# Kernel tuning notes

Hardware: AMD Instinct MI355X
Metric: run time of the kernel (lower is better)

## Reference

```python
import jax, jax.numpy as jnp
import numpy as np

N_NODES = 500_000
N_EDGES = 8_000_000
N_GRAPHS = 1000


def _mlp(x, w1, b1, w2, b2):
    # Linear -> SELU -> Linear (torch Sequential equivalent)
    return jax.nn.selu(x @ w1 + b1) @ w2 + b2


def setup_inputs() -> dict:
    key = jax.random.key(0)
    ks = jax.random.split(key, 25)
    p = lambda i, shape: jax.random.normal(ks[i], shape, jnp.float32) * 0.1
    return {
        "nodes": jax.random.normal(ks[0], (N_NODES, 1), jnp.float32),
        "edges": jax.random.normal(ks[1], (N_EDGES, 1), jnp.float32),
        "senders": jax.random.randint(ks[2], (N_EDGES,), 0, N_NODES),
        "receivers": jax.random.randint(ks[3], (N_EDGES,), 0, N_NODES),
        "graph_ids": jnp.sort(jax.random.randint(ks[4], (N_NODES,), 0, N_GRAPHS)),
        "num_graphs": N_GRAPHS,
        # permutate_nodes: 2 -> 10 -> 10
        "pn_w1": p(5, (2, 10)), "pn_b1": p(6, (10,)), "pn_w2": p(7, (10, 10)), "pn_b2": p(8, (10,)),
        # update_edges: 11 -> 5 -> 1
        "ue_w1": p(9, (11, 5)), "ue_b1": p(10, (5,)), "ue_w2": p(11, (5, 1)), "ue_b2": p(12, (1,)),
        # permutate_edges: 1 -> 5 -> 10
        "pe_w1": p(13, (1, 5)), "pe_b1": p(14, (5,)), "pe_w2": p(15, (5, 10)), "pe_b2": p(16, (10,)),
        # update_nodes: 11 -> 5 -> 1
        "un_w1": p(17, (11, 5)), "un_b1": p(18, (5,)), "un_w2": p(19, (5, 1)), "un_b2": p(20, (1,)),
        # predict: 11 -> 10 -> 10
        "pr_w1": p(21, (11, 10)), "pr_b1": p(22, (10,)), "pr_w2": p(23, (10, 10)), "pr_b2": p(24, (10,)),
    }


def reference(nodes, edges, pn_w1, pn_b1, pn_w2, pn_b2,
              ue_w1, ue_b1, ue_w2, ue_b2,
              pe_w1, pe_b1, pe_w2, pe_b2,
              un_w1, un_b1, un_w2, un_b2,
              pr_w1, pr_b1, pr_w2, pr_b2,
              senders, receivers, graph_ids, num_graphs):
    # gather node feats to edges: [recv || send] -> (E, 2)
    collected = jnp.concatenate([nodes[receivers], nodes[senders]], axis=-1)
    h1_nodes = _mlp(collected, pn_w1, pn_b1, pn_w2, pn_b2)  # (E, 10)
    h1_edges = edges  # (E, 1)
    for _ in range(3):
        h1_edges = _mlp(jnp.concatenate([h1_edges, h1_nodes], axis=-1),
                        ue_w1, ue_b1, ue_w2, ue_b2)  # (E, 1)
    # edges -> nodes aggregation (sum over receiver)
    edges_of_nodes = jax.ops.segment_sum(h1_edges, receivers, num_segments=nodes.shape[0])  # (N, 1)
    h2_edges = _mlp(edges_of_nodes, pe_w1, pe_b1, pe_w2, pe_b2)  # (N, 10)
    h2_nodes = nodes  # (N, 1)
    for _ in range(3):
        h2_nodes = _mlp(jnp.concatenate([h2_nodes, h2_edges], axis=-1),
                        un_w1, un_b1, un_w2, un_b2)  # (N, 1)
    # nodes -> globals aggregation (sum per graph)
    g = jax.ops.segment_sum(jnp.concatenate([h2_nodes, h2_edges], axis=-1),
                            graph_ids, num_segments=num_graphs)  # (G, 11)
    out = _mlp(g, pr_w1, pr_b1, pr_w2, pr_b2)  # (G, 10)
    return jax.nn.softmax(out, axis=-1)
```

## Files before the change

### kernel.cpp

```cpp
#include <hip/hip_runtime.h>
#include <hip/hip_fp16.h>
#include <math.h>

#define N_NODES_C  500000
#define N_EDGES_C  8000000
#define N_GRAPHS_C 1000
#define NGROUPS_C  (N_EDGES_C / 4)

#define BSHIFT  11
#define BWIDTH  2048
#define NBKT    245
#define BCAP    34048

#define EPB     8192
#define GPB     (EPB / 4)
#define NPB     ((N_EDGES_C + EPB - 1) / EPB)

#define GRAPH_ACC_OFF 0
#define FW_OFF        11008
#define CURSOR_OFF    11264
#define PAIRS_OFF     11520
#define WS_WORDS_NEEDED (PAIRS_OFF + NBKT * BCAP)
#define OLD_NODE_ACC_OFF 11264
#define OLD_ZERO_WORDS   (OLD_NODE_ACC_OFF + N_NODES_C)

#define LOG2E_F 1.4426950408889634f


__device__ __forceinline__ float selu2(float xl) {
    const float C1 = 0.7282901039f;
    const float C2 = 1.7580993408473766f;
    float e = __builtin_amdgcn_exp2f(xl);
    float neg = fmaf(C2, e, -C2);
    return xl > 0.0f ? C1 * xl : neg;
}

__device__ __forceinline__ float selu_f(float x) {
    const float scale = 1.0507009873554805f;
    const float sa    = 1.0507009873554805f * 1.6732632423543772f;
    float neg = sa * (__expf(x) - 1.0f);
    return x > 0.0f ? scale * x : neg;
}

__device__ __forceinline__ void atomAddF(float* p, float v) {
    __hip_atomic_fetch_add(p, v, __ATOMIC_RELAXED, __HIP_MEMORY_SCOPE_AGENT);
}

__device__ __forceinline__ void fuse_weights(
        int t,
        const float* __restrict__ pn_w1, const float* __restrict__ pn_b1,
        const float* __restrict__ pn_w2, const float* __restrict__ pn_b2,
        const float* __restrict__ ue_w1, const float* __restrict__ ue_b1,
        const float* __restrict__ ue_w2, const float* __restrict__ ue_b2,
        const float* __restrict__ pe_w1, const float* __restrict__ pe_b1,
        const float* __restrict__ pe_w2, const float* __restrict__ pe_b2,
        const float* __restrict__ un_w1, const float* __restrict__ un_b1,
        const float* __restrict__ un_w2, const float* __restrict__ un_b2,
        float* __restrict__ fw) {
    const float L = LOG2E_F;
    if (t < 20) fw[0 + t] = pn_w1[t] * L;
    if (t < 10) fw[20 + t] = pn_b1[t] * L;
    if (t < 50) {
        int j = t / 5, k = t % 5;
        float s = 0.0f;
        for (int m = 0; m < 10; ++m) s += pn_w2[j * 10 + m] * ue_w1[(1 + m) * 5 + k];
        fw[30 + t] = s * L;
    }
    if (t < 5) {
        float s = ue_b1[t];
        for (int m = 0; m < 10; ++m) s += pn_b2[m] * ue_w1[(1 + m) * 5 + t];
        fw[80 + t] = s * L;
    }
    if (t < 5)  fw[85 + t]  = ue_w1[t] * L;
    if (t < 5)  fw[90 + t]  = ue_w2[t];
    if (t == 0) fw[95]      = ue_b2[0];
    if (t < 5)  fw[96 + t]  = pe_w1[t] * L;
    if (t < 5)  fw[101 + t] = pe_b1[t] * L;
    if (t < 50) fw[106 + t] = pe_w2[t];
    if (t < 10) fw[156 + t] = pe_b2[t];
    if (t < 25) {
        int j = t / 5, k = t % 5;
        float s = 0.0f;
        for (int m = 0; m < 10; ++m) s += pe_w2[j * 10 + m] * un_w1[(1 + m) * 5 + k];
        fw[166 + t] = s * L;
    }
    if (t < 5) {
        float s = un_b1[t];
        for (int m = 0; m < 10; ++m) s += pe_b2[m] * un_w1[(1 + m) * 5 + t];
        fw[191 + t] = s * L;
    }
    if (t < 5)  fw[196 + t] = un_w1[t] * L;
    if (t < 5)  fw[201 + t] = un_w2[t];
    if (t == 0) fw[206]     = un_b2[0];
}

__global__ __launch_bounds__(256) void k_init(
        float* __restrict__ ws,
        const float* pn_w1, const float* pn_b1, const float* pn_w2, const float* pn_b2,
        const float* ue_w1, const float* ue_b1, const float* ue_w2, const float* ue_b2,
        const float* pe_w1, const float* pe_b1, const float* pe_w2, const float* pe_b2,
        const float* un_w1, const float* un_b1, const float* un_w2, const float* un_b2) {
    int i = blockIdx.x * 256 + threadIdx.x;
    if (i < 11000) ws[GRAPH_ACC_OFF + i] = 0.0f;
    if (i < 256) ((int*)ws)[CURSOR_OFF + i] = i * BCAP;
    if (blockIdx.x == 0)
        fuse_weights(threadIdx.x, pn_w1, pn_b1, pn_w2, pn_b2, ue_w1, ue_b1, ue_w2, ue_b2,
                     pe_w1, pe_b1, pe_w2, pe_b2, un_w1, un_b1, un_w2, un_b2, ws + FW_OFF);
}

__global__ void k_fuse(const float* pn_w1, const float* pn_b1, const float* pn_w2, const float* pn_b2,
                       const float* ue_w1, const float* ue_b1, const float* ue_w2, const float* ue_b2,
                       const float* pe_w1, const float* pe_b1, const float* pe_w2, const float* pe_b2,
                       const float* un_w1, const float* un_b1, const float* un_w2, const float* un_b2,
                       float* fw) {
    fuse_weights(threadIdx.x, pn_w1, pn_b1, pn_w2, pn_b2, ue_w1, ue_b1, ue_w2, ue_b2,
                 pe_w1, pe_b1, pe_w2, pe_b2, un_w1, un_b1, un_w2, un_b2, fw);
}

__global__ void k_final(const float* __restrict__ graph_acc,
                        const float* __restrict__ pr_w1, const float* __restrict__ pr_b1,
                        const float* __restrict__ pr_w2, const float* __restrict__ pr_b2,
                        float* __restrict__ out) {
    int g = blockIdx.x * blockDim.x + threadIdx.x;
    if (g >= N_GRAPHS_C) return;
    float gv[11];
#pragma unroll
    for (int f = 0; f < 11; ++f) gv[f] = graph_acc[g * 11 + f];
    float h[10];
#pragma unroll
    for (int j = 0; j < 10; ++j) {
        float z = pr_b1[j];
#pragma unroll
        for (int f = 0; f < 11; ++f) z = fmaf(gv[f], pr_w1[f * 10 + j], z);
        h[j] = selu_f(z);
    }
    float o[10];
    float mx = -1e30f;
#pragma unroll
    for (int j = 0; j < 10; ++j) {
        float z = pr_b2[j];
#pragma unroll
        for (int m = 0; m < 10; ++m) z = fmaf(h[m], pr_w2[m * 10 + j], z);
        o[j] = z;
        mx = fmaxf(mx, z);
    }
    float sum = 0.0f;
#pragma unroll
    for (int j = 0; j < 10; ++j) { o[j] = __expf(o[j] - mx); sum += o[j]; }
    float inv = 1.0f / sum;
#pragma unroll
    for (int j = 0; j < 10; ++j) out[g * 10 + j] = o[j] * inv;
}


__global__ __launch_bounds__(256) void k_part(
        const float* __restrict__ nodes, const float* __restrict__ edges,
        const int* __restrict__ senders, const int* __restrict__ receivers,
        const float* __restrict__ fw, int* __restrict__ cursor,
        unsigned int* __restrict__ pairs) {
    __shared__ int hist[256];
    __shared__ int lstart[256];
    __shared__ int cursorS[256];
    __shared__ int gbase[256];
    __shared__ unsigned int staged[EPB];

    int tid = threadIdx.x;
    int p   = blockIdx.x;
    int gstart = p * GPB;
    int gnum   = NGROUPS_C - gstart;
    if (gnum > GPB) gnum = GPB;

    hist[tid] = 0;
    __syncthreads();

    int4 rv4[8];
#pragma unroll
    for (int r = 0; r < 8; ++r) {
        int idx = r * 256 + tid;
        if (idx < gnum) {
            rv4[r] = ((const int4*)receivers)[gstart + idx];
            atomicAdd(&hist[rv4[r].x >> BSHIFT], 1);
            atomicAdd(&hist[rv4[r].y >> BSHIFT], 1);
            atomicAdd(&hist[rv4[r].z >> BSHIFT], 1);
            atomicAdd(&hist[rv4[r].w >> BSHIFT], 1);
        }
    }
    __syncthreads();

    int orig = hist[tid];
    int val  = orig;
    for (int d = 1; d < 256; d <<= 1) {
        int add = (tid >= d) ? hist[tid - d] : 0;
        __syncthreads();
        if (tid >= d) { val += add; hist[tid] = val; }
        __syncthreads();
    }
    int excl = val - orig;
    lstart[tid]  = excl;
    cursorS[tid] = excl;
    if (tid < NBKT) {
        int gb = (orig > 0)
            ? __hip_atomic_fetch_add(&cursor[tid], orig, __ATOMIC_RELAXED,
                                     __HIP_MEMORY_SCOPE_AGENT)
            : tid * BCAP;
        gbase[tid] = gb;
    }
    __syncthreads();

    float w_pn1[20], b_pn1[10], W_eb[50], b_eb[5], w1r0[5], w2e[5];
#pragma unroll
    for (int j = 0; j < 20; ++j) w_pn1[j] = fw[j];
#pragma unroll
    for (int j = 0; j < 10; ++j) b_pn1[j] = fw[20 + j];
#pragma unroll
    for (int j = 0; j < 50; ++j) W_eb[j] = fw[30 + j];
#pragma unroll
    for (int j = 0; j < 5; ++j) b_eb[j] = fw[80 + j];
#pragma unroll
    for (int j = 0; j < 5; ++j) w1r0[j] = fw[85 + j];
#pragma unroll
    for (int j = 0; j < 5; ++j) w2e[j] = fw[90 + j];
    float b2e = fw[95];

#pragma unroll
    for (int r = 0; r < 8; ++r) {
        int idx = r * 256 + tid;
        if (idx >= gnum) continue;
        int g = gstart + idx;
        float4 e4 = ((const float4*)edges)[g];
        int4  s4 = ((const int4*)senders)[g];
        float ev[4] = {e4.x, e4.y, e4.z, e4.w};
        int   sv[4] = {s4.x, s4.y, s4.z, s4.w};
        int   rv[4] = {rv4[r].x, rv4[r].y, rv4[r].z, rv4[r].w};
        float nsv[4], nrv[4];
#pragma unroll
        for (int u = 0; u < 4; ++u) { nsv[u] = nodes[sv[u]]; nrv[u] = nodes[rv[u]]; }
#pragma unroll
        for (int u = 0; u < 4; ++u) {
            float nr = nrv[u], ns = nsv[u];
            float bs[5];
#pragma unroll
            for (int k = 0; k < 5; ++k) bs[k] = b_eb[k];
#pragma unroll
            for (int j = 0; j < 10; ++j) {
                float zl = fmaf(nr, w_pn1[j], fmaf(ns, w_pn1[10 + j], b_pn1[j]));
                float sz = selu2(zl);
#pragma unroll
                for (int k = 0; k < 5; ++k) bs[k] = fmaf(sz, W_eb[j * 5 + k], bs[k]);
            }
            float e = ev[u];
#pragma unroll
            for (int it = 0; it < 3; ++it) {
                float acc2 = b2e;
#pragma unroll
                for (int k = 0; k < 5; ++k) {
                    float tt = selu2(fmaf(e, w1r0[k], bs[k]));
                    acc2 = fmaf(tt, w2e[k], acc2);
                }
                e = acc2;
            }
            int bkt  = rv[u] >> BSHIFT;
            int slot = atomicAdd(&cursorS[bkt], 1);
            unsigned int pk = ((unsigned int)(rv[u] & (BWIDTH - 1)) << 16)
                            | (unsigned int)__half_as_ushort(__float2half_rn(e));
            staged[slot] = pk;
        }
    }
    __syncthreads();

    int wv = tid >> 6, lane = tid & 63;
    for (int bkt = wv; bkt < NBKT; bkt += 4) {
        int st  = lstart[bkt];
        int cnt = hist[bkt] - st;
        int gb  = gbase[bkt];
        int lim = (bkt + 1) * BCAP;
        for (int i = lane; i < cnt; i += 64) {
            int d = gb + i;
            if (d < lim) pairs[d] = staged[st + i];
        }
    }
}

__global__ __launch_bounds__(1024) void k_gather(
        const float* __restrict__ nodes, const int* __restrict__ graph_ids,
        const float* __restrict__ fw, const int* __restrict__ cursor,
        const unsigned int* __restrict__ pairs, float* __restrict__ graph_acc) {
    __shared__ float accf[BWIDTH];
    __shared__ float garr[16 * 11];
    int tid = threadIdx.x;
    int b   = blockIdx.x;

#pragma unroll
    for (int q = 0; q < BWIDTH / 1024; ++q) accf[q * 1024 + tid] = 0.0f;
    if (tid < 176) garr[tid] = 0.0f;
    __syncthreads();

    int cnt = cursor[b] - b * BCAP;
    cnt = cnt < 0 ? 0 : (cnt > BCAP ? BCAP : cnt);

    const unsigned int* base = pairs + (size_t)b * BCAP;
    const uint4* p4 = (const uint4*)base;
    int n4 = cnt >> 2;
    for (int i = tid; i < n4; i += 1024) {
        uint4 q = p4[i];
        atomicAdd(&accf[(q.x >> 16) & (BWIDTH - 1)],
                  __half2float(__ushort_as_half((unsigned short)(q.x & 0xffff))));
        atomicAdd(&accf[(q.y >> 16) & (BWIDTH - 1)],
                  __half2float(__ushort_as_half((unsigned short)(q.y & 0xffff))));
        atomicAdd(&accf[(q.z >> 16) & (BWIDTH - 1)],
                  __half2float(__ushort_as_half((unsigned short)(q.z & 0xffff))));
        atomicAdd(&accf[(q.w >> 16) & (BWIDTH - 1)],
                  __half2float(__ushort_as_half((unsigned short)(q.w & 0xffff))));
    }
    if (tid < (cnt & 3)) {
        unsigned int q = base[(n4 << 2) + tid];
        atomicAdd(&accf[(q >> 16) & (BWIDTH - 1)],
                  __half2float(__ushort_as_half((unsigned short)(q & 0xffff))));
    }
    __syncthreads();

    float w_pe1[5], b_pe1[5], pe_w2[50], pe_b2[10], W_nb[25], b_nb[5], w1r0n[5], w2n[5];
#pragma unroll
    for (int j = 0; j < 5; ++j) w_pe1[j] = fw[96 + j];
#pragma unroll
    for (int j = 0; j < 5; ++j) b_pe1[j] = fw[101 + j];
#pragma unroll
    for (int j = 0; j < 50; ++j) pe_w2[j] = fw[106 + j];
#pragma unroll
    for (int j = 0; j < 10; ++j) pe_b2[j] = fw[156 + j];
#pragma unroll
    for (int j = 0; j < 25; ++j) W_nb[j] = fw[166 + j];
#pragma unroll
    for (int j = 0; j < 5; ++j) b_nb[j] = fw[191 + j];
#pragma unroll
    for (int j = 0; j < 5; ++j) w1r0n[j] = fw[196 + j];
#pragma unroll
    for (int j = 0; j < 5; ++j) w2n[j] = fw[201 + j];
    float b2n = fw[206];

    int gidBase = graph_ids[b << BSHIFT];

#pragma unroll
    for (int q = 0; q < BWIDTH / 1024; ++q) {
        int local = q * 1024 + tid;
        int i = (b << BSHIFT) + local;
        bool valid = i < N_NODES_C;

        float s = accf[local];
        float t5[5];
#pragma unroll
        for (int k = 0; k < 5; ++k) t5[k] = selu2(fmaf(s, w_pe1[k], b_pe1[k]));
        float he[10];
#pragma unroll
        for (int m = 0; m < 10; ++m) {
            float a = pe_b2[m];
#pragma unroll
            for (int k = 0; k < 5; ++k) a = fmaf(t5[k], pe_w2[k * 10 + m], a);
            he[m] = a;
        }
        float bs[5];
#pragma unroll
        for (int k = 0; k < 5; ++k) {
            float a = b_nb[k];
#pragma unroll
            for (int t = 0; t < 5; ++t) a = fmaf(t5[t], W_nb[t * 5 + k], a);
            bs[k] = a;
        }
        float n = valid ? nodes[i] : 0.0f;
#pragma unroll
        for (int it = 0; it < 3; ++it) {
            float a = b2n;
#pragma unroll
            for (int k = 0; k < 5; ++k) {
                float tt = selu2(fmaf(n, w1r0n[k], bs[k]));
                a = fmaf(tt, w2n[k], a);
            }
            n = a;
        }

        int gid = valid ? graph_ids[i] : -1;
        if (!valid) {
            n = 0.0f;
#pragma unroll
            for (int m = 0; m < 10; ++m) he[m] = 0.0f;
        }

        int gid0 = __shfl(gid, 0, 64);
        bool allsame = __all(gid == gid0) && (gid0 >= 0);
        if (allsame) {
            float v = n;
#pragma unroll
            for (int off = 32; off > 0; off >>= 1) v += __shfl_down(v, off, 64);
            float vh[10];
#pragma unroll
            for (int m = 0; m < 10; ++m) {
                float ww = he[m];
#pragma unroll
                for (int off = 32; off > 0; off >>= 1) ww += __shfl_down(ww, off, 64);
                vh[m] = ww;
            }
            if ((tid & 63) == 0) {
                int off = gid0 - gidBase;
                if (off >= 0 && off < 16) {
                    atomicAdd(&garr[off * 11 + 0], v);
#pragma unroll
                    for (int m = 0; m < 10; ++m) atomicAdd(&garr[off * 11 + 1 + m], vh[m]);
                } else {
                    atomAddF(&graph_acc[gid0 * 11 + 0], v);
#pragma unroll
                    for (int m = 0; m < 10; ++m) atomAddF(&graph_acc[gid0 * 11 + 1 + m], vh[m]);
                }
            }
        } else if (valid) {
            int off = gid - gidBase;
            if (off >= 0 && off < 16) {
                atomicAdd(&garr[off * 11 + 0], n);
#pragma unroll
                for (int m = 0; m < 10; ++m) atomicAdd(&garr[off * 11 + 1 + m], he[m]);
            } else {
                atomAddF(&graph_acc[gid * 11 + 0], n);
#pragma unroll
                for (int m = 0; m < 10; ++m) atomAddF(&graph_acc[gid * 11 + 1 + m], he[m]);
            }
        }
    }
    __syncthreads();

    if (tid < 176) {
        float v = garr[tid];
        if (v != 0.0f) {
            int off = tid / 11, f = tid - off * 11;
            int gg = gidBase + off;
            if (gg < N_GRAPHS_C) atomAddF(&graph_acc[gg * 11 + f], v);
        }
    }
}


__global__ __launch_bounds__(256) void k_zero(float* __restrict__ ws, int len4) {
    int i = blockIdx.x * 256 + threadIdx.x;
    if (i < len4) ((float4*)ws)[i] = make_float4(0.f, 0.f, 0.f, 0.f);
}

__global__ __launch_bounds__(256) void k_edges(
        const float* __restrict__ nodes, const float* __restrict__ edges,
        const int* __restrict__ senders, const int* __restrict__ receivers,
        const float* __restrict__ fw, float* __restrict__ node_acc) {
    float w_pn1[20], b_pn1[10], W_eb[50], b_eb[5], w1r0[5], w2e[5];
#pragma unroll
    for (int j = 0; j < 20; ++j) w_pn1[j] = fw[j];
#pragma unroll
    for (int j = 0; j < 10; ++j) b_pn1[j] = fw[20 + j];
#pragma unroll
    for (int j = 0; j < 50; ++j) W_eb[j] = fw[30 + j];
#pragma unroll
    for (int j = 0; j < 5; ++j) b_eb[j] = fw[80 + j];
#pragma unroll
    for (int j = 0; j < 5; ++j) w1r0[j] = fw[85 + j];
#pragma unroll
    for (int j = 0; j < 5; ++j) w2e[j] = fw[90 + j];
    float b2e = fw[95];

    int g = blockIdx.x * 256 + threadIdx.x;
    if (g >= N_EDGES_C / 4) return;

    float4 e4 = ((const float4*)edges)[g];
    int4  s4 = ((const int4*)senders)[g];
    int4  r4 = ((const int4*)receivers)[g];
    float ev[4] = {e4.x, e4.y, e4.z, e4.w};
    int   sv[4] = {s4.x, s4.y, s4.z, s4.w};
    int   rv[4] = {r4.x, r4.y, r4.z, r4.w};
    float nsv[4], nrv[4];
#pragma unroll
    for (int u = 0; u < 4; ++u) { nsv[u] = nodes[sv[u]]; nrv[u] = nodes[rv[u]]; }
#pragma unroll
    for (int u = 0; u < 4; ++u) {
        float nr = nrv[u], ns = nsv[u];
        float bs[5];
#pragma unroll
        for (int k = 0; k < 5; ++k) bs[k] = b_eb[k];
#pragma unroll
        for (int j = 0; j < 10; ++j) {
            float zl = fmaf(nr, w_pn1[j], fmaf(ns, w_pn1[10 + j], b_pn1[j]));
            float sz = selu2(zl);
#pragma unroll
            for (int k = 0; k < 5; ++k) bs[k] = fmaf(sz, W_eb[j * 5 + k], bs[k]);
        }
        float e = ev[u];
#pragma unroll
        for (int it = 0; it < 3; ++it) {
            float acc2 = b2e;
#pragma unroll
            for (int k = 0; k < 5; ++k) {
                float tt = selu2(fmaf(e, w1r0[k], bs[k]));
                acc2 = fmaf(tt, w2e[k], acc2);
            }
            e = acc2;
        }
        atomAddF(&node_acc[rv[u]], e);
    }
}

__global__ __launch_bounds__(256) void k_nodes(
        const float* __restrict__ nodes, const int* __restrict__ graph_ids,
        const float* __restrict__ fw, const float* __restrict__ node_acc,
        float* __restrict__ graph_acc) {
    float w_pe1[5], b_pe1[5], pe_w2[50], pe_b2[10], W_nb[25], b_nb[5], w1r0n[5], w2n[5];
#pragma unroll
    for (int j = 0; j < 5; ++j) w_pe1[j] = fw[96 + j];
#pragma unroll
    for (int j = 0; j < 5; ++j) b_pe1[j] = fw[101 + j];
#pragma unroll
    for (int j = 0; j < 50; ++j) pe_w2[j] = fw[106 + j];
#pragma unroll
    for (int j = 0; j < 10; ++j) pe_b2[j] = fw[156 + j];
#pragma unroll
    for (int j = 0; j < 25; ++j) W_nb[j] = fw[166 + j];
#pragma unroll
    for (int j = 0; j < 5; ++j) b_nb[j] = fw[191 + j];
#pragma unroll
    for (int j = 0; j < 5; ++j) w1r0n[j] = fw[196 + j];
#pragma unroll
    for (int j = 0; j < 5; ++j) w2n[j] = fw[201 + j];
    float b2n = fw[206];

    int i = blockIdx.x * 256 + threadIdx.x;
    bool valid = i < N_NODES_C;
    int ii = valid ? i : (N_NODES_C - 1);

    float s = node_acc[ii];
    float t5[5];
#pragma unroll
    for (int k = 0; k < 5; ++k) t5[k] = selu2(fmaf(s, w_pe1[k], b_pe1[k]));
    float he[10];
#pragma unroll
    for (int m = 0; m < 10; ++m) {
        float a = pe_b2[m];
#pragma unroll
        for (int k = 0; k < 5; ++k) a = fmaf(t5[k], pe_w2[k * 10 + m], a);
        he[m] = a;
    }
    float bs[5];
#pragma unroll
    for (int k = 0; k < 5; ++k) {
        float a = b_nb[k];
#pragma unroll
        for (int t = 0; t < 5; ++t) a = fmaf(t5[t], W_nb[t * 5 + k], a);
        bs[k] = a;
    }
    float n = nodes[ii];
#pragma unroll
    for (int it = 0; it < 3; ++it) {
        float a = b2n;
#pragma unroll
        for (int k = 0; k < 5; ++k) {
            float tt = selu2(fmaf(n, w1r0n[k], bs[k]));
            a = fmaf(tt, w2n[k], a);
        }
        n = a;
    }

    int gid = valid ? graph_ids[ii] : -1;
    if (!valid) {
        n = 0.0f;
#pragma unroll
        for (int m = 0; m < 10; ++m) he[m] = 0.0f;
    }

    int gid0 = __shfl(gid, 0, 64);
    bool allsame = __all(gid == gid0) && (gid0 >= 0);
    if (allsame) {
        float v = n;
#pragma unroll
        for (int off = 32; off > 0; off >>= 1) v += __shfl_down(v, off, 64);
        float vh[10];
#pragma unroll
        for (int m = 0; m < 10; ++m) {
            float ww = he[m];
#pragma unroll
            for (int off = 32; off > 0; off >>= 1) ww += __shfl_down(ww, off, 64);
            vh[m] = ww;
        }
        if ((threadIdx.x & 63) == 0) {
            atomAddF(&graph_acc[gid0 * 11 + 0], v);
#pragma unroll
            for (int m = 0; m < 10; ++m) atomAddF(&graph_acc[gid0 * 11 + 1 + m], vh[m]);
        }
    } else if (valid) {
        atomAddF(&graph_acc[gid * 11 + 0], n);
#pragma unroll
        for (int m = 0; m < 10; ++m) atomAddF(&graph_acc[gid * 11 + 1 + m], he[m]);
    }
}


extern "C" void kernel_launch(void* const* d_in, const int* in_sizes, int n_in,
                              void* d_out, int out_size, void* d_ws, size_t ws_size,
                              hipStream_t stream) {
    const float* nodes     = (const float*)d_in[0];
    const float* edges     = (const float*)d_in[1];
    const int*   senders   = (const int*)d_in[2];
    const int*   receivers = (const int*)d_in[3];
    const int*   graph_ids = (const int*)d_in[4];
    const float* pn_w1 = (const float*)d_in[6];
    const float* pn_b1 = (const float*)d_in[7];
    const float* pn_w2 = (const float*)d_in[8];
    const float* pn_b2 = (const float*)d_in[9];
    const float* ue_w1 = (const float*)d_in[10];
    const float* ue_b1 = (const float*)d_in[11];
    const float* ue_w2 = (const float*)d_in[12];
    const float* ue_b2 = (const float*)d_in[13];
    const float* pe_w1 = (const float*)d_in[14];
    const float* pe_b1 = (const float*)d_in[15];
    const float* pe_w2 = (const float*)d_in[16];
    const float* pe_b2 = (const float*)d_in[17];
    const float* un_w1 = (const float*)d_in[18];
    const float* un_b1 = (const float*)d_in[19];
    const float* un_w2 = (const float*)d_in[20];
    const float* un_b2 = (const float*)d_in[21];
    const float* pr_w1 = (const float*)d_in[22];
    const float* pr_b1 = (const float*)d_in[23];
    const float* pr_w2 = (const float*)d_in[24];
    const float* pr_b2 = (const float*)d_in[25];

    float* ws        = (float*)d_ws;
    float* graph_acc = ws + GRAPH_ACC_OFF;
    float* fw        = ws + FW_OFF;
    float* outp      = (float*)d_out;

    if (ws_size >= (size_t)WS_WORDS_NEEDED * 4) {
        int* cursor          = (int*)ws + CURSOR_OFF;
        unsigned int* pairs  = (unsigned int*)ws + PAIRS_OFF;

        hipLaunchKernelGGL(k_init, dim3(44), dim3(256), 0, stream, ws,
                           pn_w1, pn_b1, pn_w2, pn_b2, ue_w1, ue_b1, ue_w2, ue_b2,
                           pe_w1, pe_b1, pe_w2, pe_b2, un_w1, un_b1, un_w2, un_b2);
        hipLaunchKernelGGL(k_part, dim3(NPB), dim3(256), 0, stream,
                           nodes, edges, senders, receivers, fw, cursor, pairs);
        hipLaunchKernelGGL(k_gather, dim3(NBKT), dim3(1024), 0, stream,
                           nodes, graph_ids, fw, cursor, pairs, graph_acc);
        hipLaunchKernelGGL(k_final, dim3((N_GRAPHS_C + 255) / 256), dim3(256), 0, stream,
                           graph_acc, pr_w1, pr_b1, pr_w2, pr_b2, outp);
    } else {
        float* node_acc = ws + OLD_NODE_ACC_OFF;
        int len4 = OLD_ZERO_WORDS / 4;
        hipLaunchKernelGGL(k_zero, dim3((len4 + 255) / 256), dim3(256), 0, stream, ws, len4);
        hipLaunchKernelGGL(k_fuse, dim3(1), dim3(64), 0, stream,
                           pn_w1, pn_b1, pn_w2, pn_b2, ue_w1, ue_b1, ue_w2, ue_b2,
                           pe_w1, pe_b1, pe_w2, pe_b2, un_w1, un_b1, un_w2, un_b2, fw);
        hipLaunchKernelGGL(k_edges, dim3((N_EDGES_C / 4 + 255) / 256), dim3(256), 0, stream,
                           nodes, edges, senders, receivers, fw, node_acc);
        hipLaunchKernelGGL(k_nodes, dim3((N_NODES_C + 255) / 256), dim3(256), 0, stream,
                           nodes, graph_ids, fw, node_acc, graph_acc);
        hipLaunchKernelGGL(k_final, dim3((N_GRAPHS_C + 255) / 256), dim3(256), 0, stream,
                           graph_acc, pr_w1, pr_b1, pr_w2, pr_b2, outp);
    }
}
```

Before: 345.0 us.

## Split bucket gather into aggregation and node kernels, halve partition block size

The partition kernel now processes 4096 edges per block instead of 8192, so more blocks run, and it scatters staged pairs with a flat per-element binary search over the bucket histogram instead of a per-wave loop over buckets. The former fused gather kernel is split in two: k_agg writes per-node sums to a global node_acc array, and k_nodes2 runs the node MLPs and writes per-graph partials into two parity buffers without global atomics. k_final then sums graph_acc with both partial buffers. The aim is higher occupancy and less serialization in the scatter and the global atomics, at the cost of one extra launch and a round trip of node_acc through global memory.

```diff
diff --git a/kernel.cpp b/kernel.cpp
--- a/kernel.cpp
+++ b/kernel.cpp
@@ -12,17 +12,19 @@
 #define NBKT    245
 #define BCAP    34048
 
-#define EPB     8192
+#define EPB     4096
 #define GPB     (EPB / 4)
-#define NPB     ((N_EDGES_C + EPB - 1) / EPB)
+#define NPB     ((NGROUPS_C + GPB - 1) / GPB)
 
 #define GRAPH_ACC_OFF 0
-#define FW_OFF        11008
-#define CURSOR_OFF    11264
-#define PAIRS_OFF     11520
-#define WS_WORDS_NEEDED (PAIRS_OFF + NBKT * BCAP)
-#define OLD_NODE_ACC_OFF 11264
-#define OLD_ZERO_WORDS   (OLD_NODE_ACC_OFF + N_NODES_C)
+#define PARTIALS_OFF  11008
+#define FW_OFF        33024
+#define CURSOR_OFF    33280
+#define NODE_ACC_OFF  33536
+#define PAIRS_OFF     533536
+#define PAIRS_WORDS   (NBKT * BCAP)
+#define WS_WORDS_NEEDED (PAIRS_OFF + PAIRS_WORDS)
+#define ZERO_HEAD     33024
 
 #define LOG2E_F 1.4426950408889634f
 
@@ -101,7 +103,7 @@
         const float* pe_w1, const float* pe_b1, const float* pe_w2, const float* pe_b2,
         const float* un_w1, const float* un_b1, const float* un_w2, const float* un_b2) {
     int i = blockIdx.x * 256 + threadIdx.x;
-    if (i < 11000) ws[GRAPH_ACC_OFF + i] = 0.0f;
+    if (i < ZERO_HEAD) ws[i] = 0.0f;
     if (i < 256) ((int*)ws)[CURSOR_OFF + i] = i * BCAP;
     if (blockIdx.x == 0)
         fuse_weights(threadIdx.x, pn_w1, pn_b1, pn_w2, pn_b2, ue_w1, ue_b1, ue_w2, ue_b2,
@@ -118,6 +120,7 @@
 }
 
 __global__ void k_final(const float* __restrict__ graph_acc,
+                        const float* __restrict__ partials,
                         const float* __restrict__ pr_w1, const float* __restrict__ pr_b1,
                         const float* __restrict__ pr_w2, const float* __restrict__ pr_b2,
                         float* __restrict__ out) {
@@ -125,7 +128,8 @@
     if (g >= N_GRAPHS_C) return;
     float gv[11];
 #pragma unroll
-    for (int f = 0; f < 11; ++f) gv[f] = graph_acc[g * 11 + f];
+    for (int f = 0; f < 11; ++f)
+        gv[f] = graph_acc[g * 11 + f] + partials[g * 11 + f] + partials[11000 + g * 11 + f];
     float h[10];
 #pragma unroll
     for (int j = 0; j < 10; ++j) {
@@ -161,7 +165,7 @@
     __shared__ int hist[256];
     __shared__ int lstart[256];
     __shared__ int cursorS[256];
-    __shared__ int gbase[256];
+    __shared__ int delta[256];
     __shared__ unsigned int staged[EPB];
 
     int tid = threadIdx.x;
@@ -173,9 +177,9 @@
     hist[tid] = 0;
     __syncthreads();
 
-    int4 rv4[8];
-#pragma unroll
-    for (int r = 0; r < 8; ++r) {
+    int4 rv4[4];
+#pragma unroll
+    for (int r = 0; r < 4; ++r) {
         int idx = r * 256 + tid;
         if (idx < gnum) {
             rv4[r] = ((const int4*)receivers)[gstart + idx];
@@ -203,7 +207,7 @@
             ? __hip_atomic_fetch_add(&cursor[tid], orig, __ATOMIC_RELAXED,
                                      __HIP_MEMORY_SCOPE_AGENT)
             : tid * BCAP;
-        gbase[tid] = gb;
+        delta[tid] = gb - excl;
     }
     __syncthreads();
 
@@ -223,7 +227,7 @@
     float b2e = fw[95];
 
 #pragma unroll
-    for (int r = 0; r < 8; ++r) {
+    for (int r = 0; r < 4; ++r) {
         int idx = r * 256 + tid;
         if (idx >= gnum) continue;
         int g = gstart + idx;
@@ -268,31 +272,27 @@
     }
     __syncthreads();
 
-    int wv = tid >> 6, lane = tid & 63;
-    for (int bkt = wv; bkt < NBKT; bkt += 4) {
-        int st  = lstart[bkt];
-        int cnt = hist[bkt] - st;
-        int gb  = gbase[bkt];
-        int lim = (bkt + 1) * BCAP;
-        for (int i = lane; i < cnt; i += 64) {
-            int d = gb + i;
-            if (d < lim) pairs[d] = staged[st + i];
-        }
-    }
-}
-
-__global__ __launch_bounds__(1024) void k_gather(
-        const float* __restrict__ nodes, const int* __restrict__ graph_ids,
-        const float* __restrict__ fw, const int* __restrict__ cursor,
-        const unsigned int* __restrict__ pairs, float* __restrict__ graph_acc) {
+    int fe = gnum * 4;
+    for (int i = tid; i < fe; i += 256) {
+        int pos = 0;
+#pragma unroll
+        for (int s = 128; s > 0; s >>= 1) {
+            int cand = pos + s;
+            if (cand <= 255 && hist[cand - 1] <= i) pos = cand;
+        }
+        int d = i + delta[pos];
+        if (d < PAIRS_WORDS) pairs[d] = staged[i];
+    }
+}
+
+__global__ __launch_bounds__(1024) void k_agg(
+        const int* __restrict__ cursor, const unsigned int* __restrict__ pairs,
+        float* __restrict__ node_acc) {
     __shared__ float accf[BWIDTH];
-    __shared__ float garr[16 * 11];
     int tid = threadIdx.x;
     int b   = blockIdx.x;
 
-#pragma unroll
-    for (int q = 0; q < BWIDTH / 1024; ++q) accf[q * 1024 + tid] = 0.0f;
-    if (tid < 176) garr[tid] = 0.0f;
+    accf[tid] = 0.0f; accf[1024 + tid] = 0.0f;
     __syncthreads();
 
     int cnt = cursor[b] - b * BCAP;
@@ -319,6 +319,24 @@
     }
     __syncthreads();
 
+#pragma unroll
+    for (int q = 0; q < 2; ++q) {
+        int i = (b << BSHIFT) + q * 1024 + tid;
+        if (i < N_NODES_C) node_acc[i] = accf[q * 1024 + tid];
+    }
+}
+
+__global__ __launch_bounds__(1024) void k_nodes2(
+        const float* __restrict__ nodes, const int* __restrict__ graph_ids,
+        const float* __restrict__ fw, const float* __restrict__ node_acc,
+        float* __restrict__ graph_acc, float* __restrict__ partials) {
+    __shared__ float garr[32 * 11];
+    int tid = threadIdx.x;
+    int b   = blockIdx.x;
+
+    if (tid < 352) garr[tid] = 0.0f;
+    __syncthreads();
+
     float w_pe1[5], b_pe1[5], pe_w2[50], pe_b2[10], W_nb[25], b_nb[5], w1r0n[5], w2n[5];
 #pragma unroll
     for (int j = 0; j < 5; ++j) w_pe1[j] = fw[96 + j];
@@ -338,15 +356,19 @@
     for (int j = 0; j < 5; ++j) w2n[j] = fw[201 + j];
     float b2n = fw[206];
 
-    int gidBase = graph_ids[b << BSHIFT];
-
-#pragma unroll
-    for (int q = 0; q < BWIDTH / 1024; ++q) {
+    int nodeBase = b << BSHIFT;
+    int lastIdx  = nodeBase + BWIDTH;
+    if (lastIdx > N_NODES_C) lastIdx = N_NODES_C;
+    int gidBase = graph_ids[nodeBase];
+    int gidEnd  = graph_ids[lastIdx - 1];
+
+#pragma unroll
+    for (int q = 0; q < 2; ++q) {
         int local = q * 1024 + tid;
-        int i = (b << BSHIFT) + local;
+        int i = nodeBase + local;
         bool valid = i < N_NODES_C;
 
-        float s = accf[local];
+        float s = valid ? node_acc[i] : 0.0f;
         float t5[5];
 #pragma unroll
         for (int k = 0; k < 5; ++k) t5[k] = selu2(fmaf(s, w_pe1[k], b_pe1[k]));
@@ -401,7 +423,7 @@
             }
             if ((tid & 63) == 0) {
                 int off = gid0 - gidBase;
-                if (off >= 0 && off < 16) {
+                if (off >= 0 && off < 32) {
                     atomicAdd(&garr[off * 11 + 0], v);
 #pragma unroll
                     for (int m = 0; m < 10; ++m) atomicAdd(&garr[off * 11 + 1 + m], vh[m]);
@@ -413,7 +435,7 @@
             }
         } else if (valid) {
             int off = gid - gidBase;
-            if (off >= 0 && off < 16) {
+            if (off >= 0 && off < 32) {
                 atomicAdd(&garr[off * 11 + 0], n);
 #pragma unroll
                 for (int m = 0; m < 10; ++m) atomicAdd(&garr[off * 11 + 1 + m], he[m]);
@@ -426,13 +448,12 @@
     }
     __syncthreads();
 
-    if (tid < 176) {
-        float v = garr[tid];
-        if (v != 0.0f) {
-            int off = tid / 11, f = tid - off * 11;
-            int gg = gidBase + off;
-            if (gg < N_GRAPHS_C) atomAddF(&graph_acc[gg * 11 + f], v);
-        }
+    int ngl = gidEnd - gidBase + 1;
+    if (ngl > 32) ngl = 32;
+    int par = (b & 1) * 11000;
+    for (int t = tid; t < ngl * 11; t += 1024) {
+        int off = t / 11, f = t - off * 11;
+        partials[par + (gidBase + off) * 11 + f] = garr[t];
     }
 }
 
@@ -462,7 +483,7 @@
     float b2e = fw[95];
 
     int g = blockIdx.x * 256 + threadIdx.x;
-    if (g >= N_EDGES_C / 4) return;
+    if (g >= NGROUPS_C) return;
 
     float4 e4 = ((const float4*)edges)[g];
     int4  s4 = ((const int4*)senders)[g];
@@ -625,34 +646,37 @@
 
     float* ws        = (float*)d_ws;
     float* graph_acc = ws + GRAPH_ACC_OFF;
+    float* partials  = ws + PARTIALS_OFF;
     float* fw        = ws + FW_OFF;
+    float* node_acc  = ws + NODE_ACC_OFF;
     float* outp      = (float*)d_out;
 
     if (ws_size >= (size_t)WS_WORDS_NEEDED * 4) {
         int* cursor          = (int*)ws + CURSOR_OFF;
         unsigned int* pairs  = (unsigned int*)ws + PAIRS_OFF;
 
-        hipLaunchKernelGGL(k_init, dim3(44), dim3(256), 0, stream, ws,
+        hipLaunchKernelGGL(k_init, dim3((ZERO_HEAD + 255) / 256), dim3(256), 0, stream, ws,
                            pn_w1, pn_b1, pn_w2, pn_b2, ue_w1, ue_b1, ue_w2, ue_b2,
                            pe_w1, pe_b1, pe_w2, pe_b2, un_w1, un_b1, un_w2, un_b2);
         hipLaunchKernelGGL(k_part, dim3(NPB), dim3(256), 0, stream,
                            nodes, edges, senders, receivers, fw, cursor, pairs);
-        hipLaunchKernelGGL(k_gather, dim3(NBKT), dim3(1024), 0, stream,
-                           nodes, graph_ids, fw, cursor, pairs, graph_acc);
+        hipLaunchKernelGGL(k_agg, dim3(NBKT), dim3(1024), 0, stream,
+                           cursor, pairs, node_acc);
+        hipLaunchKernelGGL(k_nodes2, dim3(NBKT), dim3(1024), 0, stream,
+                           nodes, graph_ids, fw, node_acc, graph_acc, partials);
         hipLaunchKernelGGL(k_final, dim3((N_GRAPHS_C + 255) / 256), dim3(256), 0, stream,
-                           graph_acc, pr_w1, pr_b1, pr_w2, pr_b2, outp);
+                           graph_acc, partials, pr_w1, pr_b1, pr_w2, pr_b2, outp);
     } else {
-        float* node_acc = ws + OLD_NODE_ACC_OFF;
-        int len4 = OLD_ZERO_WORDS / 4;
+        int len4 = (NODE_ACC_OFF + N_NODES_C) / 4;
         hipLaunchKernelGGL(k_zero, dim3((len4 + 255) / 256), dim3(256), 0, stream, ws, len4);
         hipLaunchKernelGGL(k_fuse, dim3(1), dim3(64), 0, stream,
                            pn_w1, pn_b1, pn_w2, pn_b2, ue_w1, ue_b1, ue_w2, ue_b2,
                            pe_w1, pe_b1, pe_w2, pe_b2, un_w1, un_b1, un_w2, un_b2, fw);
-        hipLaunchKernelGGL(k_edges, dim3((N_EDGES_C / 4 + 255) / 256), dim3(256), 0, stream,
+        hipLaunchKernelGGL(k_edges, dim3((NGROUPS_C + 255) / 256), dim3(256), 0, stream,
                            nodes, edges, senders, receivers, fw, node_acc);
         hipLaunchKernelGGL(k_nodes, dim3((N_NODES_C + 255) / 256), dim3(256), 0, stream,
                            nodes, graph_ids, fw, node_acc, graph_acc);
         hipLaunchKernelGGL(k_final, dim3((N_GRAPHS_C + 255) / 256), dim3(256), 0, stream,
-                           graph_acc, pr_w1, pr_b1, pr_w2, pr_b2, outp);
-    }
-}
+                           graph_acc, partials, pr_w1, pr_b1, pr_w2, pr_b2, outp);
+    }
+}
```

Result: slower. 360.5 us (+4.5%).
